# Optimization experiments

Measured on AMD Instinct MI355X. Metric: run time of the kernel, lower is better.

Reference implementation:

```python
import jax, jax.numpy as jnp
import numpy as np
from jax import lax

VOCAB = 27
N_EMBD = 512
D_MODEL = 256
PAD_IDX = 26
OUT = 1
B, T = 256, 512


def _lstm_layer(x, w_ih, w_hh, b_ih, b_hh):
    # x: [B, T, in]; w_ih: [4H, in]; w_hh: [4H, H]
    Bb = x.shape[0]
    H = w_hh.shape[1]
    # precompute input contribution to all gates for all timesteps
    xg = jnp.einsum('bti,gi->btg', x, w_ih) + b_ih + b_hh  # [B, T, 4H]

    def step(carry, xg_t):
        h, c = carry
        g = xg_t + h @ w_hh.T  # [B, 4H]
        i, f, gg, o = jnp.split(g, 4, axis=-1)  # PyTorch gate order i,f,g,o
        i = jax.nn.sigmoid(i)
        f = jax.nn.sigmoid(f)
        gg = jnp.tanh(gg)
        o = jax.nn.sigmoid(o)
        c = f * c + i * gg
        h = o * jnp.tanh(c)
        return (h, c), h

    h0 = jnp.zeros((Bb, H), dtype=x.dtype)
    c0 = jnp.zeros((Bb, H), dtype=x.dtype)
    _, ys = lax.scan(step, (h0, c0), jnp.swapaxes(xg, 0, 1))
    return jnp.swapaxes(ys, 0, 1)  # [B, T, H]


def setup_inputs() -> dict:
    key = jax.random.key(0)
    ks = jax.random.split(key, 16)
    s_e = 1.0  # nn.Embedding default init is N(0,1)
    emb = jax.random.normal(ks[0], (VOCAB, N_EMBD), dtype=jnp.float32)
    emb = emb.at[PAD_IDX].set(0.0)
    bound = 1.0 / np.sqrt(D_MODEL)

    def u(k, shape, b):
        return jax.random.uniform(k, shape, dtype=jnp.float32, minval=-b, maxval=b)

    inp = {
        'input_ids': jax.random.randint(ks[1], (B, T), 0, VOCAB, dtype=jnp.int64)
                      if jax.config.jax_enable_x64 else
                      jax.random.randint(ks[1], (B, T), 0, VOCAB).astype(jnp.int32),
        'emb': emb,
        'w_ih0': u(ks[2], (4 * D_MODEL, N_EMBD), bound),
        'w_hh0': u(ks[3], (4 * D_MODEL, D_MODEL), bound),
        'b_ih0': u(ks[4], (4 * D_MODEL,), bound),
        'b_hh0': u(ks[5], (4 * D_MODEL,), bound),
        'w_ih1': u(ks[6], (4 * D_MODEL, D_MODEL), bound),
        'w_hh1': u(ks[7], (4 * D_MODEL, D_MODEL), bound),
        'b_ih1': u(ks[8], (4 * D_MODEL,), bound),
        'b_hh1': u(ks[9], (4 * D_MODEL,), bound),
        'fc1_w': u(ks[10], (D_MODEL // 2, D_MODEL), bound),
        'fc1_b': u(ks[11], (D_MODEL // 2,), bound),
        'fc2_w': u(ks[12], (OUT, D_MODEL // 2), 1.0 / np.sqrt(D_MODEL // 2)),
        'fc2_b': u(ks[13], (OUT,), 1.0 / np.sqrt(D_MODEL // 2)),
    }
    return inp


def reference(input_ids, emb, w_ih0, w_hh0, b_ih0, b_hh0,
              w_ih1, w_hh1, b_ih1, b_hh1, fc1_w, fc1_b, fc2_w, fc2_b):
    # embedding with padding_idx: pad row forced to zero
    table = emb.at[PAD_IDX].set(0.0)
    x = table[input_ids]  # [B, T, n_embd]
    h1 = _lstm_layer(x, w_ih0, w_hh0, b_ih0, b_hh0)   # [B, T, H]
    h2 = _lstm_layer(h1, w_ih1, w_hh1, b_ih1, b_hh1)  # [B, T, H]
    last = h2[:, -1, :]                                # [B, H]
    hidden = jax.nn.relu(last @ fc1_w.T + fc1_b)
    logits = hidden @ fc2_w.T + fc2_b                  # [B, 1]
    return logits
```

## Files before the change

kernel.cpp:

```cpp
#include <hip/hip_runtime.h>

typedef unsigned short u16;
typedef unsigned int u32;
typedef unsigned long long u64;
typedef float f32x2 __attribute__((ext_vector_type(2)));

#define BATCH 256
#define TT 512
#define HID 256
#define GATES 1024
#define NEMB 512
#define VOC 27
#define HPAD 260

__device__ __forceinline__ float bf1(u16 x){ union{u32 u; float f;} v; v.u = ((u32)x) << 16; return v.f; }
__device__ __forceinline__ u16 f2bf(float f){
  union{float f; u32 u;} v; v.f = f;
  u32 u = v.u;
  return (u16)((u + 0x7fffu + ((u >> 16) & 1u)) >> 16);
}
__device__ __forceinline__ float sigm(float x){ return 1.f / (1.f + __expf(-x)); }
__device__ __forceinline__ f32x2 lo2(float4 v){ f32x2 r; r.x = v.x; r.y = v.y; return r; }
__device__ __forceinline__ f32x2 hi2(float4 v){ f32x2 r; r.x = v.z; r.y = v.w; return r; }

__global__ void k_detect(const u16* __restrict__ b, int* __restrict__ flag) {
  int bad = 0;
  for (int k = threadIdx.x; k < 512; k += 64)
    if (((b[2 * k] >> 7) & 0xFF) >= 127) bad = 1;
  unsigned long long m = __ballot(bad);
  if (threadIdx.x == 0) flag[0] = (m != 0ULL) ? 0 : 1;
}

__global__ void k_convert(const void* __restrict__ src, float* __restrict__ dst,
                          int n, const int* __restrict__ flag) {
  int i = blockIdx.x * 256 + threadIdx.x;
  if (i >= n) return;
  dst[i] = flag[0] ? bf1(((const u16*)src)[i]) : ((const float*)src)[i];
}

__global__ void k_prep(const void* __restrict__ emb, const void* __restrict__ wih,
                       const void* __restrict__ bih, const void* __restrict__ bhh,
                       const int* __restrict__ flag, float* __restrict__ W0) {
  int idx = blockIdx.x * 256 + threadIdx.x;
  if (idx >= VOC * GATES) return;
  int v = idx >> 10, g = idx & (GATES - 1);
  int isbf = flag[0];
  float acc = isbf ? (bf1(((const u16*)bih)[g]) + bf1(((const u16*)bhh)[g]))
                   : (((const float*)bih)[g] + ((const float*)bhh)[g]);
  if (v != 26) {
    float s = 0.f;
    if (isbf) {
      const u16* e = (const u16*)emb + v * NEMB;
      const u16* w = (const u16*)wih + g * NEMB;
      for (int i = 0; i < NEMB; i++) s = fmaf(bf1(e[i]), bf1(w[i]), s);
    } else {
      const float* e = (const float*)emb + v * NEMB;
      const float* w = (const float*)wih + g * NEMB;
      for (int i = 0; i < NEMB; i++) s = fmaf(e[i], w[i], s);
    }
    acc += s;
  }
  W0[idx] = acc;
}

__global__ __launch_bounds__(1024) void k_lstm(
    const int* __restrict__ ids, const float* __restrict__ W0,
    const float* __restrict__ whh0, const float* __restrict__ wih1,
    const float* __restrict__ whh1,
    const float* __restrict__ bih1, const float* __restrict__ bhh1,
    float* __restrict__ h0a, float* __restrict__ h0b,
    float* __restrict__ h1a, float* __restrict__ h1b,
    u32* __restrict__ bar)
{
  const int tid = threadIdx.x;
  const int bid = blockIdx.x;
  const int bg = (bid >> 3) & 15;
  const int jc = (bid & 7) * 2 + (bid >> 7);

  const int tb = tid & 15;
  const int rr = tid >> 4;
  const int grow = ((rr >> 4) << 8) + (jc << 4) + (rr & 15);

  __shared__ __align__(16) float hp0[2][16][HPAD];
  __shared__ __align__(16) float hp1[16][HPAD];
  __shared__ float gs0[64][17];
  __shared__ float gs1[64][17];
  __shared__ int   ids_l[16][TT + 1];

  const float* wl0 = whh0 + (size_t)grow * HID;
  const float* wi  = wih1 + (size_t)grow * HID;
  const float* wh  = whh1 + (size_t)grow * HID;
  const float bsum = bih1[grow] + bhh1[grow];

  const int pj = tid & 15, pb = (tid >> 4) & 15;
  const int prow = (bg * 16 + pb) * HID + (jc * 16 + pj);
  float c0r = 0.f, c1r = 0.f;

  u32* cnt0 = bar + bg * 64;
  u32* cnt1 = cnt0 + 32;

  #pragma unroll
  for (int u = 0; u < 8; ++u) {
    int e = tid + 1024 * u;
    int b = e >> 9, tt = e & 511;
    ids_l[b][tt] = ids[(bg * 16 + b) * TT + tt];
  }

  for (int t = 0; t <= TT + 1; ++t) {
    if (tid == 0) {
      if (t >= 1 && t <= TT) {
        u32 want = 16u * (u32)t;
        while (__hip_atomic_load(cnt0, __ATOMIC_RELAXED, __HIP_MEMORY_SCOPE_AGENT) < want)
          __builtin_amdgcn_s_sleep(1);
      }
      if (t >= 3) {
        u32 want = 16u * (u32)(t - 2);
        while (__hip_atomic_load(cnt1, __ATOMIC_RELAXED, __HIP_MEMORY_SCOPE_AGENT) < want)
          __builtin_amdgcn_s_sleep(1);
      }
    }
    __syncthreads();

    if (t <= TT) {
      const float* h0p = ((t + 1) & 1) ? h0b : h0a;
      const u64* s0 = (const u64*)(h0p + bg * 16 * HID);
      float (*dst)[HPAD] = hp0[t & 1];
      #pragma unroll
      for (int u = 0; u < 2; ++u) {
        int e = tid + 1024 * u;
        u64 v = __hip_atomic_load(s0 + e, __ATOMIC_RELAXED, __HIP_MEMORY_SCOPE_AGENT);
        *(u64*)&dst[e >> 7][(e & 127) * 2] = v;
      }
    }
    if (t >= 2) {
      const float* h1p = ((t + 1) & 1) ? h1b : h1a;
      const u64* s1 = (const u64*)(h1p + bg * 16 * HID);
      #pragma unroll
      for (int u = 0; u < 2; ++u) {
        int e = tid + 1024 * u;
        u64 v = __hip_atomic_load(s1 + e, __ATOMIC_RELAXED, __HIP_MEMORY_SCOPE_AGENT);
        *(u64*)&hp1[e >> 7][(e & 127) * 2] = v;
      }
    }
    __syncthreads();

    if (t < TT) {
      float xgv = W0[(size_t)ids_l[tb][t] * GATES + grow];
      const float4* w4 = (const float4*)wl0;
      const float4* h4 = (const float4*)hp0[t & 1][tb];
      f32x2 sA = {0.f, 0.f}, sB = {0.f, 0.f};
      #pragma unroll 8
      for (int k = 0; k < 64; ++k) {
        float4 q = w4[k], hv = h4[k];
        sA = lo2(q) * lo2(hv) + sA;
        sB = hi2(q) * hi2(hv) + sB;
      }
      gs0[rr][tb] = xgv + sA.x + sA.y + sB.x + sB.y;
    }
    __syncthreads();

    if (t < TT && tid < 256) {
      float gi = sigm(gs0[pj][pb]);
      float gf = sigm(gs0[16 + pj][pb]);
      float gg = tanhf(gs0[32 + pj][pb]);
      float go = sigm(gs0[48 + pj][pb]);
      c0r = fmaf(gf, c0r, gi * gg);
      float* h0n = (t & 1) ? h0b : h0a;
      __hip_atomic_store(&h0n[prow], go * tanhf(c0r),
                         __ATOMIC_RELAXED, __HIP_MEMORY_SCOPE_AGENT);
    }
    __syncthreads();
    if (tid == 0 && t < TT)
      __hip_atomic_fetch_add(cnt0, 1u, __ATOMIC_RELAXED, __HIP_MEMORY_SCOPE_AGENT);

    if (t >= 2) {
      const float4* wi4 = (const float4*)wi;
      const float4* wh4 = (const float4*)wh;
      const float4* x4  = (const float4*)hp0[(t - 1) & 1][tb];
      const float4* h4  = (const float4*)hp1[tb];
      f32x2 sIa = {0.f,0.f}, sIb = {0.f,0.f}, sHa = {0.f,0.f}, sHb = {0.f,0.f};
      #pragma unroll 8
      for (int k = 0; k < 64; ++k) {
        float4 qi = wi4[k], qh = wh4[k], xv = x4[k], hv = h4[k];
        sIa = lo2(qi) * lo2(xv) + sIa;
        sIb = hi2(qi) * hi2(xv) + sIb;
        sHa = lo2(qh) * lo2(hv) + sHa;
        sHb = hi2(qh) * hi2(hv) + sHb;
      }
      gs1[rr][tb] = bsum + sIa.x + sIa.y + sIb.x + sIb.y
                         + sHa.x + sHa.y + sHb.x + sHb.y;
    }
    __syncthreads();

    if (t >= 2 && tid < 256) {
      float gi = sigm(gs1[pj][pb]);
      float gf = sigm(gs1[16 + pj][pb]);
      float gg = tanhf(gs1[32 + pj][pb]);
      float go = sigm(gs1[48 + pj][pb]);
      c1r = fmaf(gf, c1r, gi * gg);
      float* h1n = (t & 1) ? h1b : h1a;
      __hip_atomic_store(&h1n[prow], go * tanhf(c1r),
                         __ATOMIC_RELAXED, __HIP_MEMORY_SCOPE_AGENT);
    }
    __syncthreads();
    if (tid == 0 && t >= 2 && t <= TT)
      __hip_atomic_fetch_add(cnt1, 1u, __ATOMIC_RELAXED, __HIP_MEMORY_SCOPE_AGENT);
  }
}

__global__ __launch_bounds__(128) void k_fc(
    const float* __restrict__ hfin,
    const void* __restrict__ fc1w, const void* __restrict__ fc1b,
    const void* __restrict__ fc2w, const void* __restrict__ fc2b,
    const int* __restrict__ flag, void* __restrict__ out) {
  int b = blockIdx.x, j = threadIdx.x;
  __shared__ float red[128];
  const float* h = hfin + b * HID;
  int isbf = flag[0];
  float acc = isbf ? bf1(((const u16*)fc1b)[j]) : ((const float*)fc1b)[j];
  if (isbf) {
    const u16* w = (const u16*)fc1w + j * HID;
    for (int k = 0; k < HID; k++) acc = fmaf(bf1(w[k]), h[k], acc);
  } else {
    const float* w = (const float*)fc1w + j * HID;
    for (int k = 0; k < HID; k++) acc = fmaf(w[k], h[k], acc);
  }
  acc = fmaxf(acc, 0.f);
  float w2 = isbf ? bf1(((const u16*)fc2w)[j]) : ((const float*)fc2w)[j];
  red[j] = acc * w2;
  __syncthreads();
  for (int s = 64; s > 0; s >>= 1) {
    if (j < s) red[j] += red[j + s];
    __syncthreads();
  }
  if (j == 0) {
    float b2 = isbf ? bf1(((const u16*)fc2b)[0]) : ((const float*)fc2b)[0];
    float r = red[0] + b2;
    if (isbf) ((u16*)out)[b] = f2bf(r);
    else      ((float*)out)[b] = r;
  }
}

extern "C" void kernel_launch(void* const* d_in, const int* in_sizes, int n_in,
                              void* d_out, int out_size, void* d_ws, size_t ws_size,
                              hipStream_t stream) {
  const int* ids   = (const int*)d_in[0];
  const void* emb  = d_in[1];
  const void* wih0 = d_in[2];
  const void* whh0 = d_in[3];
  const void* bih0 = d_in[4];
  const void* bhh0 = d_in[5];
  const void* wih1 = d_in[6];
  const void* whh1 = d_in[7];
  const void* bih1 = d_in[8];
  const void* bhh1 = d_in[9];
  const void* fc1w = d_in[10];
  const void* fc1b = d_in[11];
  const void* fc2w = d_in[12];
  const void* fc2b = d_in[13];

  float* ws = (float*)d_ws;
  int*   flag    = (int*)ws;
  float* W0emb   = ws + 16;
  float* whh0_f  = W0emb  + VOC * GATES;
  float* wih1_f  = whh0_f + GATES * HID;
  float* whh1_f  = wih1_f + GATES * HID;
  float* bih1_f  = whh1_f + GATES * HID;
  float* bhh1_f  = bih1_f + GATES;
  float* h0A = bhh1_f + GATES;
  float* h0B = h0A + BATCH * HID;
  float* c0  = h0B + BATCH * HID;
  float* h1A = c0  + BATCH * HID;
  float* h1B = h1A + BATCH * HID;
  float* c1  = h1B + BATCH * HID;
  u32*   bar = (u32*)c0;

  k_detect<<<1, 64, 0, stream>>>((const u16*)bih0, flag);

  k_convert<<<(GATES * HID + 255) / 256, 256, 0, stream>>>(whh0, whh0_f, GATES * HID, flag);
  k_convert<<<(GATES * HID + 255) / 256, 256, 0, stream>>>(wih1, wih1_f, GATES * HID, flag);
  k_convert<<<(GATES * HID + 255) / 256, 256, 0, stream>>>(whh1, whh1_f, GATES * HID, flag);
  k_convert<<<(GATES + 255) / 256, 256, 0, stream>>>(bih1, bih1_f, GATES, flag);
  k_convert<<<(GATES + 255) / 256, 256, 0, stream>>>(bhh1, bhh1_f, GATES, flag);

  hipMemsetAsync(h0A, 0, (size_t)6 * BATCH * HID * sizeof(float), stream);

  k_prep<<<(VOC * GATES + 255) / 256, 256, 0, stream>>>(emb, wih0, bih0, bhh0, flag, W0emb);

  k_lstm<<<256, 1024, 0, stream>>>(ids, W0emb, whh0_f, wih1_f, whh1_f,
                                   bih1_f, bhh1_f, h0A, h0B, h1A, h1B, bar);

  k_fc<<<BATCH, 128, 0, stream>>>(h1B, fc1w, fc1b, fc2w, fc2b, flag, d_out);
}
```

Measured before the change: 13.10 ms.

## Regroup blocks to 4-batch x 64-unit tiles with per-block step flags

Each block now covers 4 batch rows and a quarter of the hidden units (64 units x 4 gates) instead of 16 rows x 16 units. A block then only waits on the 3 peer blocks of its batch group rather than 16. The shared atomic counters are replaced by per-block monotonic step flags on separate cache lines, polled in parallel by one wavefront. The intent is to cut cross-block synchronization latency and contention on each recurrent step. In exchange each block reads more weight rows per batch element, and the weight reuse across batch drops from 16 to 4.

```diff
diff --git a/kernel.cpp b/kernel.cpp
--- a/kernel.cpp
+++ b/kernel.cpp
@@ -74,71 +74,74 @@
 {
   const int tid = threadIdx.x;
   const int bid = blockIdx.x;
-  const int bg = (bid >> 3) & 15;
-  const int jc = (bid & 7) * 2 + (bid >> 7);
-
-  const int tb = tid & 15;
-  const int rr = tid >> 4;
-  const int grow = ((rr >> 4) << 8) + (jc << 4) + (rr & 15);
-
-  __shared__ __align__(16) float hp0[2][16][HPAD];
-  __shared__ __align__(16) float hp1[16][HPAD];
-  __shared__ float gs0[64][17];
-  __shared__ float gs1[64][17];
-  __shared__ int   ids_l[16][TT + 1];
+  const int grp = ((bid >> 3) << 1) | (bid & 1);
+  const int jq  = (bid & 7) >> 1;
+  const int wv  = tid >> 6;
+  const int ln  = tid & 63;
+
+  const int tb = tid & 3;
+  const int rr = tid >> 2;
+  const int grow = (rr >> 6) * 256 + jq * 64 + (rr & 63);
+
+  __shared__ __align__(16) float hp0[2][4][HPAD];
+  __shared__ __align__(16) float hp1[4][HPAD];
+  __shared__ float gs0[256][5];
+  __shared__ float gs1[256][5];
+  __shared__ int   ids_l[4][TT];
 
   const float* wl0 = whh0 + (size_t)grow * HID;
   const float* wi  = wih1 + (size_t)grow * HID;
   const float* wh  = whh1 + (size_t)grow * HID;
   const float bsum = bih1[grow] + bhh1[grow];
 
-  const int pj = tid & 15, pb = (tid >> 4) & 15;
-  const int prow = (bg * 16 + pb) * HID + (jc * 16 + pj);
+  const int pb = tid & 3, pj = (tid >> 2) & 63;
+  const int prow = (grp * 4 + pb) * HID + (jq * 64 + pj);
   float c0r = 0.f, c1r = 0.f;
 
-  u32* cnt0 = bar + bg * 64;
-  u32* cnt1 = cnt0 + 32;
+  u32* flags0 = bar;
+  u32* flags1 = bar + 4096;
 
   #pragma unroll
-  for (int u = 0; u < 8; ++u) {
+  for (int u = 0; u < 2; ++u) {
     int e = tid + 1024 * u;
     int b = e >> 9, tt = e & 511;
-    ids_l[b][tt] = ids[(bg * 16 + b) * TT + tt];
+    ids_l[b][tt] = ids[(grp * 4 + b) * TT + tt];
   }
 
   for (int t = 0; t <= TT + 1; ++t) {
-    if (tid == 0) {
-      if (t >= 1 && t <= TT) {
-        u32 want = 16u * (u32)t;
-        while (__hip_atomic_load(cnt0, __ATOMIC_RELAXED, __HIP_MEMORY_SCOPE_AGENT) < want)
-          __builtin_amdgcn_s_sleep(1);
-      }
-      if (t >= 3) {
-        u32 want = 16u * (u32)(t - 2);
-        while (__hip_atomic_load(cnt1, __ATOMIC_RELAXED, __HIP_MEMORY_SCOPE_AGENT) < want)
-          __builtin_amdgcn_s_sleep(1);
-      }
-    }
-    __syncthreads();
-
-    if (t <= TT) {
-      const float* h0p = ((t + 1) & 1) ? h0b : h0a;
-      const u64* s0 = (const u64*)(h0p + bg * 16 * HID);
-      float (*dst)[HPAD] = hp0[t & 1];
-      #pragma unroll
-      for (int u = 0; u < 2; ++u) {
-        int e = tid + 1024 * u;
-        u64 v = __hip_atomic_load(s0 + e, __ATOMIC_RELAXED, __HIP_MEMORY_SCOPE_AGENT);
-        *(u64*)&dst[e >> 7][(e & 127) * 2] = v;
-      }
-    }
-    if (t >= 2) {
-      const float* h1p = ((t + 1) & 1) ? h1b : h1a;
-      const u64* s1 = (const u64*)(h1p + bg * 16 * HID);
-      #pragma unroll
-      for (int u = 0; u < 2; ++u) {
-        int e = tid + 1024 * u;
-        u64 v = __hip_atomic_load(s1 + e, __ATOMIC_RELAXED, __HIP_MEMORY_SCOPE_AGENT);
+    if (wv == 0) {
+      const int q = ln & 3;
+      const int pbid = ((bid >> 3) << 3) | (q << 1) | (bid & 1);
+      u32 need = 0;
+      const u32* fp = nullptr;
+      if (ln < 4) {
+        if (q != jq && t >= 1 && t <= TT) { fp = flags0 + pbid * 16; need = (u32)t; }
+      } else if (ln < 8) {
+        if (q != jq && t >= 3) { fp = flags1 + pbid * 16; need = (u32)(t - 2); }
+      }
+      for (;;) {
+        bool ok = true;
+        if (need) ok = __hip_atomic_load(fp, __ATOMIC_RELAXED, __HIP_MEMORY_SCOPE_AGENT) >= need;
+        if (__all(ok)) break;
+        __builtin_amdgcn_s_sleep(2);
+      }
+    }
+    __syncthreads();
+
+    if (tid < 512) {
+      if (t <= TT) {
+        const float* h0p = ((t + 1) & 1) ? h0b : h0a;
+        const u64* s0 = (const u64*)h0p;
+        int e = tid;
+        u64 v = __hip_atomic_load(s0 + grp * 512 + e, __ATOMIC_RELAXED, __HIP_MEMORY_SCOPE_AGENT);
+        *(u64*)&hp0[t & 1][e >> 7][(e & 127) * 2] = v;
+      }
+    } else {
+      if (t >= 2) {
+        const float* h1p = ((t + 1) & 1) ? h1b : h1a;
+        const u64* s1 = (const u64*)h1p;
+        int e = tid - 512;
+        u64 v = __hip_atomic_load(s1 + grp * 512 + e, __ATOMIC_RELAXED, __HIP_MEMORY_SCOPE_AGENT);
         *(u64*)&hp1[e >> 7][(e & 127) * 2] = v;
       }
     }
@@ -161,9 +164,9 @@
 
     if (t < TT && tid < 256) {
       float gi = sigm(gs0[pj][pb]);
-      float gf = sigm(gs0[16 + pj][pb]);
-      float gg = tanhf(gs0[32 + pj][pb]);
-      float go = sigm(gs0[48 + pj][pb]);
+      float gf = sigm(gs0[64 + pj][pb]);
+      float gg = tanhf(gs0[128 + pj][pb]);
+      float go = sigm(gs0[192 + pj][pb]);
       c0r = fmaf(gf, c0r, gi * gg);
       float* h0n = (t & 1) ? h0b : h0a;
       __hip_atomic_store(&h0n[prow], go * tanhf(c0r),
@@ -171,7 +174,8 @@
     }
     __syncthreads();
     if (tid == 0 && t < TT)
-      __hip_atomic_fetch_add(cnt0, 1u, __ATOMIC_RELAXED, __HIP_MEMORY_SCOPE_AGENT);
+      __hip_atomic_store(flags0 + bid * 16, (u32)(t + 1),
+                         __ATOMIC_RELAXED, __HIP_MEMORY_SCOPE_AGENT);
 
     if (t >= 2) {
       const float4* wi4 = (const float4*)wi;
@@ -194,9 +198,9 @@
 
     if (t >= 2 && tid < 256) {
       float gi = sigm(gs1[pj][pb]);
-      float gf = sigm(gs1[16 + pj][pb]);
-      float gg = tanhf(gs1[32 + pj][pb]);
-      float go = sigm(gs1[48 + pj][pb]);
+      float gf = sigm(gs1[64 + pj][pb]);
+      float gg = tanhf(gs1[128 + pj][pb]);
+      float go = sigm(gs1[192 + pj][pb]);
       c1r = fmaf(gf, c1r, gi * gg);
       float* h1n = (t & 1) ? h1b : h1a;
       __hip_atomic_store(&h1n[prow], go * tanhf(c1r),
@@ -204,7 +208,8 @@
     }
     __syncthreads();
     if (tid == 0 && t >= 2 && t <= TT)
-      __hip_atomic_fetch_add(cnt1, 1u, __ATOMIC_RELAXED, __HIP_MEMORY_SCOPE_AGENT);
+      __hip_atomic_store(flags1 + bid * 16, (u32)(t - 1),
+                         __ATOMIC_RELAXED, __HIP_MEMORY_SCOPE_AGENT);
   }
 }
 
```

Result: faster. 12.44 ms (-5.0%).
